# Optimization experiments

Measured on AMD Instinct MI355X. Metric: run time of the kernel, lower is better.

## Reference

```python
import jax, jax.numpy as jnp
import numpy as np

B, N, C = 2, 32768, 512
L, H = 64, 8
DH = C // H
NB = N // L
EG_HID = 16


def setup_inputs() -> dict:
    key = jax.random.key(0)
    ks = jax.random.split(key, 12)
    x = jax.random.normal(ks[0], (B, N, C), dtype=jnp.float32)
    attn_mask = jax.random.randint(ks[1], (NB, L, L), 0, 2, dtype=jnp.int32)
    edge_feats = jax.random.normal(ks[2], (NB, L, L, 4), dtype=jnp.float32)
    s = 1.0 / np.sqrt(C)
    w_qkv = jax.random.normal(ks[3], (C, 3 * C), dtype=jnp.float32) * s
    b_qkv = jnp.zeros((3 * C,), dtype=jnp.float32)
    w_proj = jax.random.normal(ks[4], (C, C), dtype=jnp.float32) * s
    b_proj = jnp.zeros((C,), dtype=jnp.float32)
    w_eg1 = jax.random.normal(ks[5], (4, EG_HID), dtype=jnp.float32) * 0.01
    b_eg1 = jnp.zeros((EG_HID,), dtype=jnp.float32)
    w_eg2 = jax.random.normal(ks[6], (EG_HID, H), dtype=jnp.float32) * 0.01
    b_eg2 = jnp.zeros((H,), dtype=jnp.float32)
    w_blk = jax.random.normal(ks[7], (C, H), dtype=jnp.float32) * 0.01
    b_blk = jnp.zeros((H,), dtype=jnp.float32)
    return {"x": x, "attn_mask": attn_mask, "edge_feats": edge_feats,
            "w_qkv": w_qkv, "b_qkv": b_qkv, "w_proj": w_proj, "b_proj": b_proj,
            "w_eg1": w_eg1, "b_eg1": b_eg1, "w_eg2": w_eg2, "b_eg2": b_eg2,
            "w_blk": w_blk, "b_blk": b_blk}


def reference(x, attn_mask, edge_feats, w_qkv, b_qkv, w_proj, b_proj,
              w_eg1, b_eg1, w_eg2, b_eg2, w_blk, b_blk):
    scale = DH ** -0.5
    x_blk = x.reshape(B, NB, L, C)
    # bias_physics: (B, NB, L, L, 4), expanded across batch
    bias = jnp.broadcast_to(edge_feats[None], (B, NB, L, L, 4))
    idx = jnp.arange(L)
    # zero diagonal, set channel 3 of diagonal to 1
    bias = bias.at[:, :, idx, idx, :].set(0.0)
    bias = bias.at[:, :, idx, idx, 3].set(1.0)
    # mask: (B, NB, L, L); ensure each query row attends to at least itself
    mask = jnp.broadcast_to(attn_mask[None], (B, NB, L, L))
    need_diag = (mask.sum(axis=-1) < 1).astype(mask.dtype)  # (B, NB, L)
    diag = mask[:, :, idx, idx]
    mask = mask.at[:, :, idx, idx].set(jnp.maximum(diag, need_diag))
    # qkv
    qkv = x_blk @ w_qkv + b_qkv  # (B, NB, L, 3C)
    q = qkv[..., :C].reshape(B, NB, L, H, DH)
    k = qkv[..., C:2 * C].reshape(B, NB, L, H, DH)
    v = qkv[..., 2 * C:].reshape(B, NB, L, H, DH)
    scores = jnp.einsum('bnqhd,bnkhd->bnqkh', q, k) * scale
    scores = scores + bias[..., 3:4]
    mask_e = (mask[..., None] == 0)  # (B, NB, L, L, 1)
    scores = jnp.where(mask_e, -jnp.inf, scores)
    attn_probs = jax.nn.softmax(scores, axis=3)
    # edge-gate MLP: 4 -> 16 (exact GELU) -> H
    gate = jax.nn.gelu(bias @ w_eg1 + b_eg1, approximate=False) @ w_eg2 + b_eg2
    gate = jnp.where(mask_e, 0.0, gate)
    combined = attn_probs + gate
    x_mid = jnp.einsum('bnqkh,bnkhd->bnqhd', combined, v)  # (B, NB, L, H, DH)
    # block route token
    block_node = x_blk.mean(axis=2, keepdims=True)  # (B, NB, 1, C)
    v_block = (block_node @ w_qkv + b_qkv)[..., 2 * C:].reshape(B, NB, 1, H, DH)
    g_block = jax.nn.sigmoid(x_blk @ w_blk + b_blk)  # (B, NB, L, H)
    x_mid = x_mid + g_block[..., None] * v_block
    out = x_mid.reshape(B, NB, L, C) @ w_proj + b_proj
    return out.reshape(B, N, C)
```

## Files before the change

kernel.cpp:

```cpp
#include <hip/hip_runtime.h>

typedef unsigned short u16;
typedef __attribute__((ext_vector_type(8))) short bf16x8;
typedef __attribute__((ext_vector_type(4))) float f32x4;

#define NTOK 32768
#define CC 512
#define HH 8
#define LL 64
#define NBLK 512
#define MTOK 65536

__device__ __forceinline__ u16 f2bf(float f) {
    unsigned int u = __float_as_uint(f);
    unsigned int r = u + 0x7fffu + ((u >> 16) & 1u);
    return (u16)(r >> 16);
}
__device__ __forceinline__ float bf2f(u16 h) {
    return __uint_as_float(((unsigned int)h) << 16);
}
__device__ __forceinline__ bf16x8 bc8(uint4 v) {
    return __builtin_bit_cast(bf16x8, v);
}
__device__ __forceinline__ void dma16(const u16* g, u16* l) {
    __builtin_amdgcn_global_load_lds((const __attribute__((address_space(1))) void*)g,
                                     (__attribute__((address_space(3))) void*)l, 16, 0, 0);
}

__global__ __launch_bounds__(256) void convert_gblock_kernel(const float* __restrict__ x,
                                                             u16* __restrict__ xbf,
                                                             const float* __restrict__ w_blk,
                                                             const float* __restrict__ b_blk,
                                                             float* __restrict__ gbl) {
    __shared__ float wbs[4608];
    int tid = threadIdx.x;
    for (int i = tid; i < 4096; i += 256) wbs[i + (i >> 6)] = w_blk[i];
    size_t tok = (size_t)blockIdx.x * 4 + (tid >> 6);
    int lane = tid & 63;
    int c0 = lane * 8;
    const float4* p = (const float4*)(x + tok * CC + c0);
    float4 a = p[0], b = p[1];
    uint4 o;
    o.x = (unsigned)f2bf(a.x) | ((unsigned)f2bf(a.y) << 16);
    o.y = (unsigned)f2bf(a.z) | ((unsigned)f2bf(a.w) << 16);
    o.z = (unsigned)f2bf(b.x) | ((unsigned)f2bf(b.y) << 16);
    o.w = (unsigned)f2bf(b.z) | ((unsigned)f2bf(b.w) << 16);
    *(uint4*)(xbf + tok * CC + c0) = o;
    float xv[8] = {a.x, a.y, a.z, a.w, b.x, b.y, b.z, b.w};
    __syncthreads();
    float acc[8];
#pragma unroll
    for (int h = 0; h < 8; ++h) acc[h] = 0.f;
#pragma unroll
    for (int j = 0; j < 8; ++j) {
        const float* wr = &wbs[(c0 + j) * 8 + lane];
#pragma unroll
        for (int h = 0; h < 8; ++h) acc[h] += xv[j] * wr[h];
    }
#pragma unroll
    for (int h = 0; h < 8; ++h) {
#pragma unroll
        for (int off = 1; off < 64; off <<= 1) acc[h] += __shfl_xor(acc[h], off);
    }
    float v = acc[0];
#pragma unroll
    for (int h = 1; h < 8; ++h) v = (lane == h) ? acc[h] : v;
    if (lane < 8) gbl[tok * 8 + lane] = 1.f / (1.f + __expf(-(v + b_blk[lane])));
}

__global__ __launch_bounds__(256) void transpose_bf16_kernel(const float* __restrict__ in,
                                                             u16* __restrict__ out,
                                                             int K, int Nn) {
    __shared__ float tile[32][33];
    int n0 = blockIdx.x * 32, k0 = blockIdx.y * 32;
    int tx = threadIdx.x & 31, ty = threadIdx.x >> 5;
#pragma unroll
    for (int i = 0; i < 4; ++i)
        tile[ty + i * 8][tx] = in[(size_t)(k0 + ty + i * 8) * Nn + n0 + tx];
    __syncthreads();
#pragma unroll
    for (int i = 0; i < 4; ++i)
        out[(size_t)(n0 + ty + i * 8) * K + k0 + tx] = f2bf(tile[tx][ty + i * 8]);
}

__global__ __launch_bounds__(256) void gate_sbias_kernel(const int* __restrict__ mask,
                                                         const float* __restrict__ edge,
                                                         const float* __restrict__ w1,
                                                         const float* __restrict__ b1,
                                                         const float* __restrict__ w2,
                                                         const float* __restrict__ b2,
                                                         u16* __restrict__ gate2,
                                                         u16* __restrict__ sbias2) {
    __shared__ float w1s[64], b1s[16], w2s[128], b2s[8];
    __shared__ int nds[16];
    int t = threadIdx.x;
    int nb = blockIdx.x >> 2;
    int qt = blockIdx.x & 3;
    if (t < 64) w1s[t] = w1[t];
    if (t < 16) b1s[t] = b1[t];
    if (t < 128) w2s[t] = w2[t];
    if (t < 8) b2s[t] = b2[t];
    if (t >= 128 && t < 144) {
        int q = qt * 16 + (t - 128);
        int s = 0;
        const int* mr = mask + (size_t)(nb * 64 + q) * 64;
#pragma unroll 8
        for (int k = 0; k < 64; ++k) s += mr[k];
        nds[t - 128] = (s < 1) ? 1 : 0;
    }
    __syncthreads();
#pragma unroll 1
    for (int it = 0; it < 4; ++it) {
        int p = it * 256 + t;
        int ql = p >> 6, k = p & 63;
        int q = qt * 16 + ql;
        int pk = (k & 15) * 4 + (k >> 4);
        int mv = mask[(size_t)(nb * 64 + q) * 64 + k];
        float e0, e1, e2, e3;
        if (q == k) {
            mv = max(mv, nds[ql]);
            e0 = e1 = e2 = 0.f;
            e3 = 1.f;
        } else {
            const float* ep = edge + ((size_t)(nb * 64 + q) * 64 + k) * 4;
            e0 = ep[0]; e1 = ep[1]; e2 = ep[2]; e3 = ep[3];
        }
        sbias2[(size_t)(nb * 64 + q) * 64 + pk] = f2bf(mv ? e3 : -1e30f);
        float g[8];
#pragma unroll
        for (int hh = 0; hh < 8; ++hh) g[hh] = b2s[hh];
#pragma unroll
        for (int j = 0; j < 16; ++j) {
            float hpre = e0 * w1s[j] + e1 * w1s[16 + j] + e2 * w1s[32 + j] + e3 * w1s[48 + j] + b1s[j];
            float hg = 0.5f * hpre * (1.f + erff(hpre * 0.70710678f));
#pragma unroll
            for (int hh = 0; hh < 8; ++hh) g[hh] += hg * w2s[j * 8 + hh];
        }
#pragma unroll
        for (int hh = 0; hh < 8; ++hh)
            gate2[(((size_t)nb * 8 + hh) * 64 + q) * 64 + pk] = f2bf(mv ? g[hh] : 0.f);
    }
}

__global__ __launch_bounds__(256) void qkv_gemm_kernel(const u16* __restrict__ xbf,
                                                       const u16* __restrict__ wqkvT,
                                                       const float* __restrict__ b_qkv,
                                                       u16* __restrict__ qkv) {
    __shared__ __align__(16) u16 As[128 * 64], Bs[128 * 64];
    int tid = threadIdx.x;
    int flat = blockIdx.x;
    int logical = (flat & 7) * 768 + (flat >> 3);
    int n0 = (logical % 12) * 128;
    int m0 = (logical / 12) * 128;
    int lane = tid & 63, l15 = lane & 15, quad = lane >> 4, wave = tid >> 6;
    int r8 = lane >> 3, jch = lane & 7;
    int js = jch ^ r8;
    int mwl = (wave >> 1) * 64, nwl = (wave & 1) * 64;
    int sw = l15 & 7;

    f32x4 acc[4][4];
#pragma unroll
    for (int i = 0; i < 4; ++i)
#pragma unroll
        for (int j = 0; j < 4; ++j) acc[i][j] = (f32x4){0.f, 0.f, 0.f, 0.f};

    int arow[4], brow[4];
#pragma unroll
    for (int i = 0; i < 4; ++i) arow[i] = (mwl + i * 16 + l15) * 64;
#pragma unroll
    for (int j = 0; j < 4; ++j) brow[j] = (nwl + j * 16 + l15) * 64;

    const u16* gA = xbf + (size_t)(m0 + wave * 32 + r8) * CC + js * 8;
    const u16* gB = wqkvT + (size_t)(n0 + wave * 32 + r8) * CC + js * 8;
    u16* lA = As + wave * 32 * 64;
    u16* lB = Bs + wave * 32 * 64;

    for (int kt = 0; kt < 8; ++kt) {
        int k0 = kt * 64;
#pragma unroll
        for (int t = 0; t < 4; ++t) {
            dma16(gA + (size_t)t * 8 * CC + k0, lA + t * 8 * 64);
            dma16(gB + (size_t)t * 8 * CC + k0, lB + t * 8 * 64);
        }
        __syncthreads();
#pragma unroll
        for (int kk = 0; kk < 2; ++kk) {
            int ch = ((kk * 4 + quad) ^ sw) * 8;
            bf16x8 a[4], bb[4];
#pragma unroll
            for (int i = 0; i < 4; ++i) a[i] = *(const bf16x8*)&As[arow[i] + ch];
#pragma unroll
            for (int j = 0; j < 4; ++j) bb[j] = *(const bf16x8*)&Bs[brow[j] + ch];
#pragma unroll
            for (int i = 0; i < 4; ++i)
#pragma unroll
                for (int j = 0; j < 4; ++j)
                    acc[i][j] = __builtin_amdgcn_mfma_f32_16x16x32_bf16(a[i], bb[j], acc[i][j], 0, 0, 0);
        }
        __syncthreads();
    }
#pragma unroll
    for (int i = 0; i < 4; ++i)
#pragma unroll
        for (int j = 0; j < 4; ++j) {
            int col = n0 + nwl + j * 16 + l15;
            int plane = col >> 6;
            int d = col & 63;
            float bp = b_qkv[col];
#pragma unroll
            for (int r = 0; r < 4; ++r) {
                int row = m0 + mwl + i * 16 + quad * 4 + r;
                qkv[((size_t)plane * MTOK + row) * 64 + d] = f2bf(acc[i][j][r] + bp);
            }
        }
}

__global__ __launch_bounds__(256) void outproj_kernel(const u16* __restrict__ xmid,
                                                      const u16* __restrict__ wprojT,
                                                      const float* __restrict__ b_proj,
                                                      float* __restrict__ out) {
    __shared__ __align__(16) u16 As[128 * 64], Bs[128 * 64];
    int tid = threadIdx.x;
    int flat = blockIdx.x;
    int logical = (flat & 7) * 256 + (flat >> 3);
    int n0 = (logical & 3) * 128;
    int m0 = (logical >> 2) * 128;
    int lane = tid & 63, l15 = lane & 15, quad = lane >> 4, wave = tid >> 6;
    int r8 = lane >> 3, jch = lane & 7;
    int js = jch ^ r8;
    int mwl = (wave >> 1) * 64, nwl = (wave & 1) * 64;
    int sw = l15 & 7;

    f32x4 acc[4][4];
#pragma unroll
    for (int i = 0; i < 4; ++i)
#pragma unroll
        for (int j = 0; j < 4; ++j) acc[i][j] = (f32x4){0.f, 0.f, 0.f, 0.f};

    int arow[4], brow[4];
#pragma unroll
    for (int i = 0; i < 4; ++i) arow[i] = (mwl + i * 16 + l15) * 64;
#pragma unroll
    for (int j = 0; j < 4; ++j) brow[j] = (nwl + j * 16 + l15) * 64;

    const u16* gA = xmid + (size_t)(m0 + wave * 32 + r8) * CC + js * 8;
    const u16* gB = wprojT + (size_t)(n0 + wave * 32 + r8) * CC + js * 8;
    u16* lA = As + wave * 32 * 64;
    u16* lB = Bs + wave * 32 * 64;

    for (int kt = 0; kt < 8; ++kt) {
        int k0 = kt * 64;
#pragma unroll
        for (int t = 0; t < 4; ++t) {
            dma16(gA + (size_t)t * 8 * CC + k0, lA + t * 8 * 64);
            dma16(gB + (size_t)t * 8 * CC + k0, lB + t * 8 * 64);
        }
        __syncthreads();
#pragma unroll
        for (int kk = 0; kk < 2; ++kk) {
            int ch = ((kk * 4 + quad) ^ sw) * 8;
            bf16x8 a[4], bb[4];
#pragma unroll
            for (int i = 0; i < 4; ++i) a[i] = *(const bf16x8*)&As[arow[i] + ch];
#pragma unroll
            for (int j = 0; j < 4; ++j) bb[j] = *(const bf16x8*)&Bs[brow[j] + ch];
#pragma unroll
            for (int i = 0; i < 4; ++i)
#pragma unroll
                for (int j = 0; j < 4; ++j)
                    acc[i][j] = __builtin_amdgcn_mfma_f32_16x16x32_bf16(a[i], bb[j], acc[i][j], 0, 0, 0);
        }
        __syncthreads();
    }
#pragma unroll
    for (int i = 0; i < 4; ++i)
#pragma unroll
        for (int j = 0; j < 4; ++j) {
            int col = n0 + nwl + j * 16 + l15;
            float bp = b_proj[col];
#pragma unroll
            for (int r = 0; r < 4; ++r) {
                int row = m0 + mwl + i * 16 + quad * 4 + r;
                out[(size_t)row * CC + col] = acc[i][j][r] + bp;
            }
        }
}

__global__ __launch_bounds__(256) void attn_kernel(const u16* __restrict__ qkv,
                                                   const u16* __restrict__ sbias2,
                                                   const u16* __restrict__ gate2,
                                                   const float* __restrict__ gbl,
                                                   u16* __restrict__ xmid) {
    __shared__ u16 VT[64 * 72], Ps[64 * 72];
    __shared__ float gl[64], vbl[64];
    int tid = threadIdx.x;
    int bid = blockIdx.x;
    int h = bid & 7, nb = (bid >> 3) & 511, b = bid >> 12;
    int lane = tid & 63, l15 = lane & 15, quad = lane >> 4, wave = tid >> 6;
    int m0 = wave * 16;
    size_t blockrow = (size_t)(b * NTOK + nb * 64);
    const u16* qq = qkv + ((size_t)h * MTOK + blockrow) * 64;
    const u16* qk = qq + (size_t)8 * MTOK * 64;
    const u16* qv = qq + (size_t)16 * MTOK * 64;

    {
        int key = tid & 63, d0 = (tid >> 6) * 16;
        const uint4* vsrc = (const uint4*)(qv + (size_t)key * 64 + d0);
        uint4 v0 = vsrc[0], v1 = vsrc[1];
        u16 tmp[16];
        *(uint4*)tmp = v0;
        *(uint4*)(tmp + 8) = v1;
#pragma unroll
        for (int j = 0; j < 16; ++j) VT[(d0 + j) * 72 + key] = tmp[j];
    }
    if (tid < 64) gl[tid] = gbl[(blockrow + tid) * 8 + h];
    __syncthreads();

    if (tid < 64) {
        float s = 0.f;
#pragma unroll 8
        for (int k = 0; k < 64; ++k) s += bf2f(VT[tid * 72 + k]);
        vbl[tid] = s * 0.015625f;
    }

    f32x4 sc[4];
#pragma unroll
    for (int t = 0; t < 4; ++t) sc[t] = (f32x4){0.f, 0.f, 0.f, 0.f};
#pragma unroll
    for (int kk = 0; kk < 2; ++kk) {
        bf16x8 a = bc8(*(const uint4*)(qq + (size_t)(m0 + l15) * 64 + kk * 32 + quad * 8));
#pragma unroll
        for (int t = 0; t < 4; ++t) {
            bf16x8 bb = bc8(*(const uint4*)(qk + (size_t)(t * 16 + l15) * 64 + kk * 32 + quad * 8));
            sc[t] = __builtin_amdgcn_mfma_f32_16x16x32_bf16(a, bb, sc[t], 0, 0, 0);
        }
    }
    {
        const u16* sb2 = sbias2 + (size_t)nb * 4096;
        const u16* gp2 = gate2 + ((size_t)nb * 8 + h) * 4096;
#pragma unroll
        for (int r = 0; r < 4; ++r) {
            int q = m0 + quad * 4 + r;
            ushort4 sv = *(const ushort4*)(sb2 + (q * 16 + l15) * 4);
            float bias_t[4] = {bf2f(sv.x), bf2f(sv.y), bf2f(sv.z), bf2f(sv.w)};
            float mx = -3e38f;
#pragma unroll
            for (int t = 0; t < 4; ++t) {
                float v = sc[t][r] * 0.125f + bias_t[t];
                sc[t][r] = v;
                mx = fmaxf(mx, v);
            }
            mx = fmaxf(mx, __shfl_xor(mx, 1));
            mx = fmaxf(mx, __shfl_xor(mx, 2));
            mx = fmaxf(mx, __shfl_xor(mx, 4));
            mx = fmaxf(mx, __shfl_xor(mx, 8));
            float sum = 0.f;
#pragma unroll
            for (int t = 0; t < 4; ++t) {
                float p = __expf(sc[t][r] - mx);
                sc[t][r] = p;
                sum += p;
            }
            sum += __shfl_xor(sum, 1);
            sum += __shfl_xor(sum, 2);
            sum += __shfl_xor(sum, 4);
            sum += __shfl_xor(sum, 8);
            float inv = 1.f / sum;
            ushort4 gv = *(const ushort4*)(gp2 + (q * 16 + l15) * 4);
            float gate_t[4] = {bf2f(gv.x), bf2f(gv.y), bf2f(gv.z), bf2f(gv.w)};
#pragma unroll
            for (int t = 0; t < 4; ++t) {
                float comb = sc[t][r] * inv + gate_t[t];
                Ps[q * 72 + t * 16 + l15] = f2bf(comb);
            }
        }
    }
    __syncthreads();

    f32x4 o[4];
#pragma unroll
    for (int t = 0; t < 4; ++t) o[t] = (f32x4){0.f, 0.f, 0.f, 0.f};
#pragma unroll
    for (int kk = 0; kk < 2; ++kk) {
        bf16x8 a = *(const bf16x8*)&Ps[(m0 + l15) * 72 + kk * 32 + quad * 8];
#pragma unroll
        for (int t = 0; t < 4; ++t) {
            bf16x8 bb = *(const bf16x8*)&VT[(t * 16 + l15) * 72 + kk * 32 + quad * 8];
            o[t] = __builtin_amdgcn_mfma_f32_16x16x32_bf16(a, bb, o[t], 0, 0, 0);
        }
    }
#pragma unroll
    for (int t = 0; t < 4; ++t) {
#pragma unroll
        for (int r = 0; r < 4; ++r) {
            int q = m0 + quad * 4 + r, d = t * 16 + l15;
            float v = o[t][r] + gl[q] * vbl[d];
            xmid[(blockrow + q) * CC + h * 64 + d] = f2bf(v);
        }
    }
}

extern "C" void kernel_launch(void* const* d_in, const int* in_sizes, int n_in,
                              void* d_out, int out_size, void* d_ws, size_t ws_size,
                              hipStream_t stream) {
    const float* x = (const float*)d_in[0];
    const int* attn_mask = (const int*)d_in[1];
    const float* edge = (const float*)d_in[2];
    const float* w_qkv = (const float*)d_in[3];
    const float* b_qkv = (const float*)d_in[4];
    const float* w_proj = (const float*)d_in[5];
    const float* b_proj = (const float*)d_in[6];
    const float* w_eg1 = (const float*)d_in[7];
    const float* b_eg1 = (const float*)d_in[8];
    const float* w_eg2 = (const float*)d_in[9];
    const float* b_eg2 = (const float*)d_in[10];
    const float* w_blk = (const float*)d_in[11];
    const float* b_blk = (const float*)d_in[12];
    float* out = (float*)d_out;

    char* ws = (char*)d_ws;
    u16* xbf = (u16*)ws;
    u16* xmid = (u16*)ws;
    u16* qkv = (u16*)(ws + 67108864);
    u16* gate2 = (u16*)(ws + 268435456);
    u16* sbias2 = (u16*)(ws + 301989888);
    u16* wqkvT = (u16*)(ws + 306184192);
    u16* wprojT = (u16*)(ws + 307757056);
    float* gbl = (float*)(ws + 308281344);

    convert_gblock_kernel<<<16384, 256, 0, stream>>>(x, xbf, w_blk, b_blk, gbl);
    transpose_bf16_kernel<<<dim3(48, 16), 256, 0, stream>>>(w_qkv, wqkvT, 512, 1536);
    transpose_bf16_kernel<<<dim3(16, 16), 256, 0, stream>>>(w_proj, wprojT, 512, 512);
    gate_sbias_kernel<<<2048, 256, 0, stream>>>(attn_mask, edge, w_eg1, b_eg1, w_eg2, b_eg2,
                                                gate2, sbias2);
    qkv_gemm_kernel<<<6144, 256, 0, stream>>>(xbf, wqkvT, b_qkv, qkv);
    attn_kernel<<<8192, 256, 0, stream>>>(qkv, sbias2, gate2, gbl, xmid);
    outproj_kernel<<<2048, 256, 0, stream>>>(xmid, wprojT, b_proj, out);
}
```

Measured before the change: 700.3 us.

## Fuse QKV projection into attention kernel, keeping Q/K/V in shared memory

Replaces the separate QKV GEMM and attention kernels with one kernel per (batch, block, head-pair) that computes Q, K, V for its 64 tokens and two heads, stages them in LDS, and runs the attention there. This removes the round trip of the bf16 QKV tensor (about 200 MB written and read back) and one launch. In exchange, the weight B-operand is read straight from global memory without LDS staging, and each workgroup re-reads the 64x512 x tile for every head pair, so the GEMM has much less reuse. The x tile is double-buffered in LDS, and xmid moves to a separate workspace region.

```diff
diff --git a/kernel.cpp b/kernel.cpp
--- a/kernel.cpp
+++ b/kernel.cpp
@@ -142,77 +142,178 @@
     }
 }
 
-__global__ __launch_bounds__(256) void qkv_gemm_kernel(const u16* __restrict__ xbf,
-                                                       const u16* __restrict__ wqkvT,
-                                                       const float* __restrict__ b_qkv,
-                                                       u16* __restrict__ qkv) {
-    __shared__ __align__(16) u16 As[128 * 64], Bs[128 * 64];
+__global__ __launch_bounds__(512, 4) void fused_qkv_attn_kernel(const u16* __restrict__ xbf,
+                                                                const u16* __restrict__ wqkvT,
+                                                                const float* __restrict__ b_qkv,
+                                                                const u16* __restrict__ sbias2,
+                                                                const u16* __restrict__ gate2,
+                                                                const float* __restrict__ gbl,
+                                                                u16* __restrict__ xmid) {
+    __shared__ __align__(16) u16 Xs[2][64 * 64];
+    __shared__ __align__(16) u16 QPs[2][64 * 72];
+    __shared__ __align__(16) u16 Ks[2][64 * 72];
+    __shared__ __align__(16) u16 VTs[2][64 * 72];
+    __shared__ float gl[2][64], vbl[2][64];
+
     int tid = threadIdx.x;
-    int flat = blockIdx.x;
-    int logical = (flat & 7) * 768 + (flat >> 3);
-    int n0 = (logical % 12) * 128;
-    int m0 = (logical / 12) * 128;
-    int lane = tid & 63, l15 = lane & 15, quad = lane >> 4, wave = tid >> 6;
-    int r8 = lane >> 3, jch = lane & 7;
-    int js = jch ^ r8;
-    int mwl = (wave >> 1) * 64, nwl = (wave & 1) * 64;
+    int bidf = blockIdx.x;
+    int logical = (bidf & 7) * 512 + (bidf >> 3);
+    int hp = logical & 3, nb = (logical >> 2) & 511, b = logical >> 11;
+    int wave = tid >> 6, lane = tid & 63, l15 = lane & 15, quad = lane >> 4;
+    int hloc = wave >> 2;
+    int h = hp * 2 + hloc;
+    int nt = wave & 3;
+    int m0 = nt * 16;
+    size_t blockrow = (size_t)(b * NTOK + nb * 64);
+
+    int srow = tid >> 3;
+    int jch = tid & 7;
+    int js = jch ^ (srow & 7);
+    const u16* gA = xbf + (blockrow + srow) * CC + js * 8;
     int sw = l15 & 7;
 
-    f32x4 acc[4][4];
-#pragma unroll
-    for (int i = 0; i < 4; ++i)
-#pragma unroll
-        for (int j = 0; j < 4; ++j) acc[i][j] = (f32x4){0.f, 0.f, 0.f, 0.f};
-
-    int arow[4], brow[4];
-#pragma unroll
-    for (int i = 0; i < 4; ++i) arow[i] = (mwl + i * 16 + l15) * 64;
-#pragma unroll
-    for (int j = 0; j < 4; ++j) brow[j] = (nwl + j * 16 + l15) * 64;
-
-    const u16* gA = xbf + (size_t)(m0 + wave * 32 + r8) * CC + js * 8;
-    const u16* gB = wqkvT + (size_t)(n0 + wave * 32 + r8) * CC + js * 8;
-    u16* lA = As + wave * 32 * 64;
-    u16* lB = Bs + wave * 32 * 64;
-
+    const u16* gB0 = wqkvT + (size_t)(0 * 512 + h * 64 + nt * 16 + l15) * CC;
+    const u16* gB1 = wqkvT + (size_t)(1 * 512 + h * 64 + nt * 16 + l15) * CC;
+    const u16* gB2 = wqkvT + (size_t)(2 * 512 + h * 64 + nt * 16 + l15) * CC;
+    float bq0 = b_qkv[0 * 512 + h * 64 + nt * 16 + l15];
+    float bq1 = b_qkv[1 * 512 + h * 64 + nt * 16 + l15];
+    float bq2 = b_qkv[2 * 512 + h * 64 + nt * 16 + l15];
+
+    f32x4 accQ[4], accK[4], accV[4];
+#pragma unroll
+    for (int i = 0; i < 4; ++i) {
+        accQ[i] = (f32x4){0.f, 0.f, 0.f, 0.f};
+        accK[i] = (f32x4){0.f, 0.f, 0.f, 0.f};
+        accV[i] = (f32x4){0.f, 0.f, 0.f, 0.f};
+    }
+
+    dma16(gA, &Xs[0][wave * 512]);
+    __syncthreads();
     for (int kt = 0; kt < 8; ++kt) {
-        int k0 = kt * 64;
-#pragma unroll
-        for (int t = 0; t < 4; ++t) {
-            dma16(gA + (size_t)t * 8 * CC + k0, lA + t * 8 * 64);
-            dma16(gB + (size_t)t * 8 * CC + k0, lB + t * 8 * 64);
-        }
-        __syncthreads();
+        int buf = kt & 1;
+        if (kt < 7) dma16(gA + (kt + 1) * 64, &Xs[buf ^ 1][wave * 512]);
 #pragma unroll
         for (int kk = 0; kk < 2; ++kk) {
             int ch = ((kk * 4 + quad) ^ sw) * 8;
-            bf16x8 a[4], bb[4];
-#pragma unroll
-            for (int i = 0; i < 4; ++i) a[i] = *(const bf16x8*)&As[arow[i] + ch];
-#pragma unroll
-            for (int j = 0; j < 4; ++j) bb[j] = *(const bf16x8*)&Bs[brow[j] + ch];
-#pragma unroll
-            for (int i = 0; i < 4; ++i)
-#pragma unroll
-                for (int j = 0; j < 4; ++j)
-                    acc[i][j] = __builtin_amdgcn_mfma_f32_16x16x32_bf16(a[i], bb[j], acc[i][j], 0, 0, 0);
+            bf16x8 a[4];
+#pragma unroll
+            for (int i = 0; i < 4; ++i) a[i] = *(const bf16x8*)&Xs[buf][(i * 16 + l15) * 64 + ch];
+            int ko = kt * 64 + kk * 32 + quad * 8;
+            bf16x8 b0 = bc8(*(const uint4*)(gB0 + ko));
+            bf16x8 b1 = bc8(*(const uint4*)(gB1 + ko));
+            bf16x8 b2 = bc8(*(const uint4*)(gB2 + ko));
+#pragma unroll
+            for (int i = 0; i < 4; ++i) {
+                accQ[i] = __builtin_amdgcn_mfma_f32_16x16x32_bf16(a[i], b0, accQ[i], 0, 0, 0);
+                accK[i] = __builtin_amdgcn_mfma_f32_16x16x32_bf16(a[i], b1, accK[i], 0, 0, 0);
+                accV[i] = __builtin_amdgcn_mfma_f32_16x16x32_bf16(a[i], b2, accV[i], 0, 0, 0);
+            }
         }
         __syncthreads();
     }
-#pragma unroll
-    for (int i = 0; i < 4; ++i)
-#pragma unroll
-        for (int j = 0; j < 4; ++j) {
-            int col = n0 + nwl + j * 16 + l15;
-            int plane = col >> 6;
-            int d = col & 63;
-            float bp = b_qkv[col];
+
+    {
+        int dloc = nt * 16 + l15;
+#pragma unroll
+        for (int i = 0; i < 4; ++i) {
 #pragma unroll
             for (int r = 0; r < 4; ++r) {
-                int row = m0 + mwl + i * 16 + quad * 4 + r;
-                qkv[((size_t)plane * MTOK + row) * 64 + d] = f2bf(acc[i][j][r] + bp);
-            }
-        }
+                int tok = i * 16 + quad * 4 + r;
+                QPs[hloc][tok * 72 + dloc] = f2bf(accQ[i][r] + bq0);
+                Ks[hloc][tok * 72 + dloc] = f2bf(accK[i][r] + bq1);
+                VTs[hloc][dloc * 72 + tok] = f2bf(accV[i][r] + bq2);
+            }
+        }
+    }
+    if (tid < 128) {
+        int hl = tid >> 6, tok = tid & 63;
+        gl[hl][tok] = gbl[(blockrow + tok) * 8 + hp * 2 + hl];
+    }
+    __syncthreads();
+
+    if (tid < 128) {
+        int hl = tid >> 6, d = tid & 63;
+        float s = 0.f;
+#pragma unroll 8
+        for (int k = 0; k < 64; ++k) s += bf2f(VTs[hl][d * 72 + k]);
+        vbl[hl][d] = s * 0.015625f;
+    }
+
+    f32x4 sc[4];
+#pragma unroll
+    for (int t = 0; t < 4; ++t) sc[t] = (f32x4){0.f, 0.f, 0.f, 0.f};
+#pragma unroll
+    for (int kk = 0; kk < 2; ++kk) {
+        bf16x8 a = *(const bf16x8*)&QPs[hloc][(m0 + l15) * 72 + kk * 32 + quad * 8];
+#pragma unroll
+        for (int t = 0; t < 4; ++t) {
+            bf16x8 bb = *(const bf16x8*)&Ks[hloc][(t * 16 + l15) * 72 + kk * 32 + quad * 8];
+            sc[t] = __builtin_amdgcn_mfma_f32_16x16x32_bf16(a, bb, sc[t], 0, 0, 0);
+        }
+    }
+    {
+        const u16* sb2 = sbias2 + (size_t)nb * 4096;
+        const u16* gp2 = gate2 + ((size_t)nb * 8 + h) * 4096;
+#pragma unroll
+        for (int r = 0; r < 4; ++r) {
+            int q = m0 + quad * 4 + r;
+            ushort4 sv = *(const ushort4*)(sb2 + (q * 16 + l15) * 4);
+            float bias_t[4] = {bf2f(sv.x), bf2f(sv.y), bf2f(sv.z), bf2f(sv.w)};
+            float mx = -3e38f;
+#pragma unroll
+            for (int t = 0; t < 4; ++t) {
+                float v = sc[t][r] * 0.125f + bias_t[t];
+                sc[t][r] = v;
+                mx = fmaxf(mx, v);
+            }
+            mx = fmaxf(mx, __shfl_xor(mx, 1));
+            mx = fmaxf(mx, __shfl_xor(mx, 2));
+            mx = fmaxf(mx, __shfl_xor(mx, 4));
+            mx = fmaxf(mx, __shfl_xor(mx, 8));
+            float sum = 0.f;
+#pragma unroll
+            for (int t = 0; t < 4; ++t) {
+                float p = __expf(sc[t][r] - mx);
+                sc[t][r] = p;
+                sum += p;
+            }
+            sum += __shfl_xor(sum, 1);
+            sum += __shfl_xor(sum, 2);
+            sum += __shfl_xor(sum, 4);
+            sum += __shfl_xor(sum, 8);
+            float inv = 1.f / sum;
+            ushort4 gv = *(const ushort4*)(gp2 + (q * 16 + l15) * 4);
+            float gate_t[4] = {bf2f(gv.x), bf2f(gv.y), bf2f(gv.z), bf2f(gv.w)};
+#pragma unroll
+            for (int t = 0; t < 4; ++t) {
+                float comb = sc[t][r] * inv + gate_t[t];
+                QPs[hloc][q * 72 + t * 16 + l15] = f2bf(comb);
+            }
+        }
+    }
+    __syncthreads();
+
+    f32x4 o[4];
+#pragma unroll
+    for (int t = 0; t < 4; ++t) o[t] = (f32x4){0.f, 0.f, 0.f, 0.f};
+#pragma unroll
+    for (int kk = 0; kk < 2; ++kk) {
+        bf16x8 a = *(const bf16x8*)&QPs[hloc][(m0 + l15) * 72 + kk * 32 + quad * 8];
+#pragma unroll
+        for (int t = 0; t < 4; ++t) {
+            bf16x8 bb = *(const bf16x8*)&VTs[hloc][(t * 16 + l15) * 72 + kk * 32 + quad * 8];
+            o[t] = __builtin_amdgcn_mfma_f32_16x16x32_bf16(a, bb, o[t], 0, 0, 0);
+        }
+    }
+#pragma unroll
+    for (int t = 0; t < 4; ++t) {
+#pragma unroll
+        for (int r = 0; r < 4; ++r) {
+            int q = m0 + quad * 4 + r, d = t * 16 + l15;
+            float v = o[t][r] + gl[hloc][q] * vbl[hloc][d];
+            xmid[(blockrow + q) * CC + h * 64 + d] = f2bf(v);
+        }
+    }
 }
 
 __global__ __launch_bounds__(256) void outproj_kernel(const u16* __restrict__ xmid,
@@ -284,120 +385,6 @@
                 out[(size_t)row * CC + col] = acc[i][j][r] + bp;
             }
         }
-}
-
-__global__ __launch_bounds__(256) void attn_kernel(const u16* __restrict__ qkv,
-                                                   const u16* __restrict__ sbias2,
-                                                   const u16* __restrict__ gate2,
-                                                   const float* __restrict__ gbl,
-                                                   u16* __restrict__ xmid) {
-    __shared__ u16 VT[64 * 72], Ps[64 * 72];
-    __shared__ float gl[64], vbl[64];
-    int tid = threadIdx.x;
-    int bid = blockIdx.x;
-    int h = bid & 7, nb = (bid >> 3) & 511, b = bid >> 12;
-    int lane = tid & 63, l15 = lane & 15, quad = lane >> 4, wave = tid >> 6;
-    int m0 = wave * 16;
-    size_t blockrow = (size_t)(b * NTOK + nb * 64);
-    const u16* qq = qkv + ((size_t)h * MTOK + blockrow) * 64;
-    const u16* qk = qq + (size_t)8 * MTOK * 64;
-    const u16* qv = qq + (size_t)16 * MTOK * 64;
-
-    {
-        int key = tid & 63, d0 = (tid >> 6) * 16;
-        const uint4* vsrc = (const uint4*)(qv + (size_t)key * 64 + d0);
-        uint4 v0 = vsrc[0], v1 = vsrc[1];
-        u16 tmp[16];
-        *(uint4*)tmp = v0;
-        *(uint4*)(tmp + 8) = v1;
-#pragma unroll
-        for (int j = 0; j < 16; ++j) VT[(d0 + j) * 72 + key] = tmp[j];
-    }
-    if (tid < 64) gl[tid] = gbl[(blockrow + tid) * 8 + h];
-    __syncthreads();
-
-    if (tid < 64) {
-        float s = 0.f;
-#pragma unroll 8
-        for (int k = 0; k < 64; ++k) s += bf2f(VT[tid * 72 + k]);
-        vbl[tid] = s * 0.015625f;
-    }
-
-    f32x4 sc[4];
-#pragma unroll
-    for (int t = 0; t < 4; ++t) sc[t] = (f32x4){0.f, 0.f, 0.f, 0.f};
-#pragma unroll
-    for (int kk = 0; kk < 2; ++kk) {
-        bf16x8 a = bc8(*(const uint4*)(qq + (size_t)(m0 + l15) * 64 + kk * 32 + quad * 8));
-#pragma unroll
-        for (int t = 0; t < 4; ++t) {
-            bf16x8 bb = bc8(*(const uint4*)(qk + (size_t)(t * 16 + l15) * 64 + kk * 32 + quad * 8));
-            sc[t] = __builtin_amdgcn_mfma_f32_16x16x32_bf16(a, bb, sc[t], 0, 0, 0);
-        }
-    }
-    {
-        const u16* sb2 = sbias2 + (size_t)nb * 4096;
-        const u16* gp2 = gate2 + ((size_t)nb * 8 + h) * 4096;
-#pragma unroll
-        for (int r = 0; r < 4; ++r) {
-            int q = m0 + quad * 4 + r;
-            ushort4 sv = *(const ushort4*)(sb2 + (q * 16 + l15) * 4);
-            float bias_t[4] = {bf2f(sv.x), bf2f(sv.y), bf2f(sv.z), bf2f(sv.w)};
-            float mx = -3e38f;
-#pragma unroll
-            for (int t = 0; t < 4; ++t) {
-                float v = sc[t][r] * 0.125f + bias_t[t];
-                sc[t][r] = v;
-                mx = fmaxf(mx, v);
-            }
-            mx = fmaxf(mx, __shfl_xor(mx, 1));
-            mx = fmaxf(mx, __shfl_xor(mx, 2));
-            mx = fmaxf(mx, __shfl_xor(mx, 4));
-            mx = fmaxf(mx, __shfl_xor(mx, 8));
-            float sum = 0.f;
-#pragma unroll
-            for (int t = 0; t < 4; ++t) {
-                float p = __expf(sc[t][r] - mx);
-                sc[t][r] = p;
-                sum += p;
-            }
-            sum += __shfl_xor(sum, 1);
-            sum += __shfl_xor(sum, 2);
-            sum += __shfl_xor(sum, 4);
-            sum += __shfl_xor(sum, 8);
-            float inv = 1.f / sum;
-            ushort4 gv = *(const ushort4*)(gp2 + (q * 16 + l15) * 4);
-            float gate_t[4] = {bf2f(gv.x), bf2f(gv.y), bf2f(gv.z), bf2f(gv.w)};
-#pragma unroll
-            for (int t = 0; t < 4; ++t) {
-                float comb = sc[t][r] * inv + gate_t[t];
-                Ps[q * 72 + t * 16 + l15] = f2bf(comb);
-            }
-        }
-    }
-    __syncthreads();
-
-    f32x4 o[4];
-#pragma unroll
-    for (int t = 0; t < 4; ++t) o[t] = (f32x4){0.f, 0.f, 0.f, 0.f};
-#pragma unroll
-    for (int kk = 0; kk < 2; ++kk) {
-        bf16x8 a = *(const bf16x8*)&Ps[(m0 + l15) * 72 + kk * 32 + quad * 8];
-#pragma unroll
-        for (int t = 0; t < 4; ++t) {
-            bf16x8 bb = *(const bf16x8*)&VT[(t * 16 + l15) * 72 + kk * 32 + quad * 8];
-            o[t] = __builtin_amdgcn_mfma_f32_16x16x32_bf16(a, bb, o[t], 0, 0, 0);
-        }
-    }
-#pragma unroll
-    for (int t = 0; t < 4; ++t) {
-#pragma unroll
-        for (int r = 0; r < 4; ++r) {
-            int q = m0 + quad * 4 + r, d = t * 16 + l15;
-            float v = o[t][r] + gl[q] * vbl[d];
-            xmid[(blockrow + q) * CC + h * 64 + d] = f2bf(v);
-        }
-    }
 }
 
 extern "C" void kernel_launch(void* const* d_in, const int* in_sizes, int n_in,
@@ -420,8 +407,7 @@
 
     char* ws = (char*)d_ws;
     u16* xbf = (u16*)ws;
-    u16* xmid = (u16*)ws;
-    u16* qkv = (u16*)(ws + 67108864);
+    u16* xmid = (u16*)(ws + 67108864);
     u16* gate2 = (u16*)(ws + 268435456);
     u16* sbias2 = (u16*)(ws + 301989888);
     u16* wqkvT = (u16*)(ws + 306184192);
@@ -433,7 +419,6 @@
     transpose_bf16_kernel<<<dim3(16, 16), 256, 0, stream>>>(w_proj, wprojT, 512, 512);
     gate_sbias_kernel<<<2048, 256, 0, stream>>>(attn_mask, edge, w_eg1, b_eg1, w_eg2, b_eg2,
                                                 gate2, sbias2);
-    qkv_gemm_kernel<<<6144, 256, 0, stream>>>(xbf, wqkvT, b_qkv, qkv);
-    attn_kernel<<<8192, 256, 0, stream>>>(qkv, sbias2, gate2, gbl, xmid);
+    fused_qkv_attn_kernel<<<4096, 512, 0, stream>>>(xbf, wqkvT, b_qkv, sbias2, gate2, gbl, xmid);
     outproj_kernel<<<2048, 256, 0, stream>>>(xmid, wprojT, b_proj, out);
 }
```

Result: faster. 628.7 us (-10.2%).
